# Kernel tuning notes

Hardware: AMD Instinct MI355X
Metric: run time of the kernel (lower is better)

Reference implementation:

```python
import jax, jax.numpy as jnp
import numpy as np

B, S, H, D = 2, 4096, 32, 128  # batch, seq_len, num_heads, key_size
BLOCK = 128                     # block_size (S must be divisible)


def setup_inputs() -> dict:
    key = jax.random.key(0)
    kq, kk, kv = jax.random.split(key, 3)
    q = jax.random.normal(kq, (B, S, H * D), dtype=jnp.float32)
    k = jax.random.normal(kk, (B, S, H * D), dtype=jnp.float32)
    v = jax.random.normal(kv, (B, S, H * D), dtype=jnp.float32)
    return {"q": q, "k": k, "v": v}


def reference(q, k, v):
    batch, seq_len, _ = q.shape
    nb = seq_len // BLOCK  # num_blocks
    # reshape to [B, nb, block, H, D]
    qb = q.reshape(batch, nb, BLOCK, H, D)
    kb = k.reshape(batch, nb, BLOCK, H, D)
    vb = v.reshape(batch, nb, BLOCK, H, D)
    scale = np.float32(1.0 / np.sqrt(D))
    # Faithful to original einsum '...hd,...kd->...hk': contraction is over d
    # with (nb, block) as batch dims, so attention runs over the HEAD axis (g).
    logits = jnp.einsum("bnshd,bnsgd->bnshg", qb, kb) * scale  # [B,nb,block,H,H]
    w = jax.nn.softmax(logits, axis=-1)
    out = jnp.einsum("bnshg,bnsgd->bnshd", w, vb)  # [B,nb,block,H,D]
    return out.reshape(batch, seq_len, H * D)
```

## Files before the change

kernel.cpp:

```cpp
#include <hip/hip_runtime.h>


typedef __bf16 bf16x8 __attribute__((ext_vector_type(8)));
typedef __bf16 bf16x2 __attribute__((ext_vector_type(2)));
typedef float  f32x4  __attribute__((ext_vector_type(4)));

static constexpr float kScale = 0.08838834764831845f;

__global__ __launch_bounds__(256) void attn_headwise(
    const float* __restrict__ q, const float* __restrict__ k,
    const float* __restrict__ v, float* __restrict__ out, int ntok) {
  const int wave = threadIdx.x >> 6;
  const int lane = threadIdx.x & 63;
  const int lr   = lane & 15;
  const int G    = lane >> 4;

  const long token = (long)blockIdx.x * 4 + wave;
  if (token >= ntok) return;
  const float* qt = q + token * 4096;
  const float* kt = k + token * 4096;
  const float* vt = v + token * 4096;
  float*       ot = out + token * 4096;

  __shared__ __align__(16) unsigned int pbuf[4][32 * 16];
  unsigned int* pl = pbuf[wave];

  f32x4 acc[2][2];
  acc[0][0] = 0.f; acc[0][1] = 0.f; acc[1][0] = 0.f; acc[1][1] = 0.f;

  #pragma unroll
  for (int kk = 0; kk < 4; ++kk) {
    bf16x8 af[2], bq[2];
    #pragma unroll
    for (int gi = 0; gi < 2; ++gi) {
      const float* p = kt + (16 * gi + lr) * 128 + 32 * kk + 8 * G;
      f32x4 u0 = *(const f32x4*)p;
      f32x4 u1 = *(const f32x4*)(p + 4);
      bf16x8 f;
      f[0] = (__bf16)u0[0]; f[1] = (__bf16)u0[1];
      f[2] = (__bf16)u0[2]; f[3] = (__bf16)u0[3];
      f[4] = (__bf16)u1[0]; f[5] = (__bf16)u1[1];
      f[6] = (__bf16)u1[2]; f[7] = (__bf16)u1[3];
      af[gi] = f;
    }
    #pragma unroll
    for (int hj = 0; hj < 2; ++hj) {
      const float* p = qt + (16 * hj + lr) * 128 + 32 * kk + 8 * G;
      f32x4 u0 = *(const f32x4*)p;
      f32x4 u1 = *(const f32x4*)(p + 4);
      bf16x8 f;
      f[0] = (__bf16)u0[0]; f[1] = (__bf16)u0[1];
      f[2] = (__bf16)u0[2]; f[3] = (__bf16)u0[3];
      f[4] = (__bf16)u1[0]; f[5] = (__bf16)u1[1];
      f[6] = (__bf16)u1[2]; f[7] = (__bf16)u1[3];
      bq[hj] = f;
    }
    #pragma unroll
    for (int gi = 0; gi < 2; ++gi)
      #pragma unroll
      for (int hj = 0; hj < 2; ++hj)
        acc[gi][hj] = __builtin_amdgcn_mfma_f32_16x16x32_bf16(
            af[gi], bq[hj], acc[gi][hj], 0, 0, 0);
  }

  #pragma unroll
  for (int hj = 0; hj < 2; ++hj) {
    float m = acc[0][hj][0];
    #pragma unroll
    for (int gi = 0; gi < 2; ++gi)
      #pragma unroll
      for (int r = 0; r < 4; ++r) m = fmaxf(m, acc[gi][hj][r]);
    m = fmaxf(m, __shfl_xor(m, 16, 64));
    m = fmaxf(m, __shfl_xor(m, 32, 64));

    float pv[2][4];
    float s = 0.f;
    #pragma unroll
    for (int gi = 0; gi < 2; ++gi)
      #pragma unroll
      for (int r = 0; r < 4; ++r) {
        float e = __expf((acc[gi][hj][r] - m) * kScale);
        pv[gi][r] = e;
        s += e;
      }
    s += __shfl_xor(s, 16, 64);
    s += __shfl_xor(s, 32, 64);
    float inv = 1.0f / s;

    #pragma unroll
    for (int gi = 0; gi < 2; ++gi)
      #pragma unroll
      for (int mp = 0; mp < 2; ++mp) {
        bf16x2 t;
        t[0] = (__bf16)(pv[gi][2 * mp]     * inv);
        t[1] = (__bf16)(pv[gi][2 * mp + 1] * inv);
        pl[(16 * hj + lr) * 16 + 8 * gi + 2 * G + mp] =
            __builtin_bit_cast(unsigned int, t);
      }
  }

  bf16x8 pf[2];
  #pragma unroll
  for (int ht = 0; ht < 2; ++ht)
    pf[ht] = *(const bf16x8*)&pl[(16 * ht + lr) * 16 + 4 * G];

  f32x4 zero = 0.f;
  #pragma unroll
  for (int dt = 0; dt < 8; ++dt) {
    const float* vp = vt + 8 * G * 128 + 16 * dt + lr;
    bf16x8 vf;
    #pragma unroll
    for (int e = 0; e < 8; ++e) vf[e] = (__bf16)vp[e * 128];
    f32x4 o0 = __builtin_amdgcn_mfma_f32_16x16x32_bf16(vf, pf[0], zero, 0, 0, 0);
    f32x4 o1 = __builtin_amdgcn_mfma_f32_16x16x32_bf16(vf, pf[1], zero, 0, 0, 0);
    *(f32x4*)&ot[lr * 128 + 16 * dt + 4 * G]        = o0;
    *(f32x4*)&ot[(16 + lr) * 128 + 16 * dt + 4 * G] = o1;
  }
}

extern "C" void kernel_launch(void* const* d_in, const int* in_sizes, int n_in,
                              void* d_out, int out_size, void* d_ws, size_t ws_size,
                              hipStream_t stream) {
  const float* q = (const float*)d_in[0];
  const float* k = (const float*)d_in[1];
  const float* v = (const float*)d_in[2];
  float* out = (float*)d_out;
  int ntok = in_sizes[0] / 4096;
  int grid = (ntok + 3) / 4;
  hipLaunchKernelGGL(attn_headwise, dim3(grid), dim3(256), 0, stream,
                     q, k, v, out, ntok);
}
```

Measured before the change: 113.4 us.

## Prefetch Q/K into registers and stream V to LDS via direct global-to-LDS loads

All Q and K fragments for the token are loaded into registers up front instead of being loaded per k-step. V is copied into a per-wave LDS buffer with global_load_lds, issued before the QK^T and softmax phase, so the V fetch overlaps that compute and the strided scalar V gathers become LDS reads. A launch-bounds occupancy hint is added as well. The cost is 64KB of LDS per block and higher register pressure, which limits occupancy. There is also a possible LDS bank-conflict pattern on the strided V reads.

```diff
diff --git a/kernel.cpp b/kernel.cpp
--- a/kernel.cpp
+++ b/kernel.cpp
@@ -7,7 +7,19 @@
 
 static constexpr float kScale = 0.08838834764831845f;
 
-__global__ __launch_bounds__(256) void attn_headwise(
+typedef const __attribute__((address_space(1))) unsigned int* gas_ptr;
+typedef __attribute__((address_space(3))) unsigned int* las_ptr;
+
+__device__ inline bf16x8 to_bf16x8(f32x4 a, f32x4 b) {
+  bf16x8 f;
+  f[0] = (__bf16)a[0]; f[1] = (__bf16)a[1];
+  f[2] = (__bf16)a[2]; f[3] = (__bf16)a[3];
+  f[4] = (__bf16)b[0]; f[5] = (__bf16)b[1];
+  f[6] = (__bf16)b[2]; f[7] = (__bf16)b[3];
+  return f;
+}
+
+__global__ __launch_bounds__(256, 2) void attn_headwise(
     const float* __restrict__ q, const float* __restrict__ k,
     const float* __restrict__ v, float* __restrict__ out, int ntok) {
   const int wave = threadIdx.x >> 6;
@@ -22,38 +34,41 @@
   const float* vt = v + token * 4096;
   float*       ot = out + token * 4096;
 
+  __shared__ __align__(16) float        vbuf[4][32 * 128];
   __shared__ __align__(16) unsigned int pbuf[4][32 * 16];
+  float*        vl = vbuf[wave];
   unsigned int* pl = pbuf[wave];
+
+  f32x4 kraw[4][2][2], qraw[4][2][2];
+  #pragma unroll
+  for (int kk = 0; kk < 4; ++kk)
+    #pragma unroll
+    for (int t = 0; t < 2; ++t) {
+      const float* pk = kt + (16 * t + lr) * 128 + 32 * kk + 8 * G;
+      kraw[kk][t][0] = *(const f32x4*)pk;
+      kraw[kk][t][1] = *(const f32x4*)(pk + 4);
+      const float* pq = qt + (16 * t + lr) * 128 + 32 * kk + 8 * G;
+      qraw[kk][t][0] = *(const f32x4*)pq;
+      qraw[kk][t][1] = *(const f32x4*)(pq + 4);
+    }
+
+  {
+    const float* vsrc = vt + lane * 4;
+    #pragma unroll
+    for (int i = 0; i < 16; ++i)
+      __builtin_amdgcn_global_load_lds((gas_ptr)(vsrc + i * 256),
+                                       (las_ptr)(vl + i * 256), 16, 0, 0);
+  }
 
   f32x4 acc[2][2];
   acc[0][0] = 0.f; acc[0][1] = 0.f; acc[1][0] = 0.f; acc[1][1] = 0.f;
-
   #pragma unroll
   for (int kk = 0; kk < 4; ++kk) {
     bf16x8 af[2], bq[2];
     #pragma unroll
-    for (int gi = 0; gi < 2; ++gi) {
-      const float* p = kt + (16 * gi + lr) * 128 + 32 * kk + 8 * G;
-      f32x4 u0 = *(const f32x4*)p;
-      f32x4 u1 = *(const f32x4*)(p + 4);
-      bf16x8 f;
-      f[0] = (__bf16)u0[0]; f[1] = (__bf16)u0[1];
-      f[2] = (__bf16)u0[2]; f[3] = (__bf16)u0[3];
-      f[4] = (__bf16)u1[0]; f[5] = (__bf16)u1[1];
-      f[6] = (__bf16)u1[2]; f[7] = (__bf16)u1[3];
-      af[gi] = f;
-    }
-    #pragma unroll
-    for (int hj = 0; hj < 2; ++hj) {
-      const float* p = qt + (16 * hj + lr) * 128 + 32 * kk + 8 * G;
-      f32x4 u0 = *(const f32x4*)p;
-      f32x4 u1 = *(const f32x4*)(p + 4);
-      bf16x8 f;
-      f[0] = (__bf16)u0[0]; f[1] = (__bf16)u0[1];
-      f[2] = (__bf16)u0[2]; f[3] = (__bf16)u0[3];
-      f[4] = (__bf16)u1[0]; f[5] = (__bf16)u1[1];
-      f[6] = (__bf16)u1[2]; f[7] = (__bf16)u1[3];
-      bq[hj] = f;
+    for (int t = 0; t < 2; ++t) {
+      af[t] = to_bf16x8(kraw[kk][t][0], kraw[kk][t][1]);
+      bq[t] = to_bf16x8(qraw[kk][t][0], qraw[kk][t][1]);
     }
     #pragma unroll
     for (int gi = 0; gi < 2; ++gi)
@@ -104,13 +119,14 @@
   for (int ht = 0; ht < 2; ++ht)
     pf[ht] = *(const bf16x8*)&pl[(16 * ht + lr) * 16 + 4 * G];
 
+  asm volatile("s_waitcnt vmcnt(0)" ::: "memory");
   f32x4 zero = 0.f;
   #pragma unroll
   for (int dt = 0; dt < 8; ++dt) {
-    const float* vp = vt + 8 * G * 128 + 16 * dt + lr;
     bf16x8 vf;
     #pragma unroll
-    for (int e = 0; e < 8; ++e) vf[e] = (__bf16)vp[e * 128];
+    for (int e = 0; e < 8; ++e)
+      vf[e] = (__bf16)vl[(8 * G + e) * 128 + 16 * dt + lr];
     f32x4 o0 = __builtin_amdgcn_mfma_f32_16x16x32_bf16(vf, pf[0], zero, 0, 0, 0);
     f32x4 o1 = __builtin_amdgcn_mfma_f32_16x16x32_bf16(vf, pf[1], zero, 0, 0, 0);
     *(f32x4*)&ot[lr * 128 + 16 * dt + 4 * G]        = o0;
```

Result: no change. 113.3 us, median of 2 (-0.1%).
